# Optimization experiments

Hardware: AMD Instinct MI355X
Metric: run time of the kernel (lower is better)

The kernel has to match this reference:

```python
import jax, jax.numpy as jnp
import numpy as np

N_NODES = 100000
NNZ = 1600000
IN_CH = 256
OUT_CH = 64  # heads * out_channels, heads=1


def setup_inputs() -> dict:
    key = jax.random.key(0)
    k1, k2, k3, k4, k5 = jax.random.split(key, 5)
    X = jax.random.normal(k1, (N_NODES, IN_CH), dtype=jnp.float32)
    # nn.Linear(in, heads*out, bias=False) weight: [out, in]
    W_lin = jax.random.normal(k2, (OUT_CH, IN_CH), dtype=jnp.float32) * (1.0 / np.sqrt(IN_CH))
    # sparse Laplacian L in COO form
    L_rows = jax.random.randint(k3, (NNZ,), 0, N_NODES, dtype=jnp.int64)
    L_cols = jax.random.randint(k4, (NNZ,), 0, N_NODES, dtype=jnp.int64)
    L_vals = jax.random.uniform(k5, (NNZ,), dtype=jnp.float32)
    return {"g1": 0, "g2": 0, "X": X, "W_lin": W_lin,
            "L_rows": L_rows, "L_cols": L_cols, "L_vals": L_vals}


def reference(g1, g2, X, W_lin, L_rows, L_cols, L_vals):
    # dense projection: X @ W^T  -> [N, out]
    Xp = jnp.einsum('ni,oi->no', X, W_lin)
    # SpMM: Xv = L @ Xp, COO gather-scale-scatter
    gathered = L_vals[:, None] * Xp[L_cols]            # [nnz, out]
    Xv = jax.ops.segment_sum(gathered, L_rows, num_segments=N_NODES)
    return Xv
```

## Files before the change

### kernel.cpp

```cpp
#include <hip/hip_runtime.h>

#define N_IN_CH 256
#define N_OUT_CH 64
#define XPAD 264
#define BROW 128
#define NBK 1024
#define B1_T 256
#define B1_E 2048
#define ECAP 4096
#define OVFCAP 65536
#define NGEMM 512

typedef __attribute__((ext_vector_type(8))) short short8;
typedef __attribute__((ext_vector_type(4))) float f32x4;

__device__ inline ushort f2bf(float f) {
    unsigned u = __float_as_uint(f);
    return (ushort)((u + 0x7FFFu + ((u >> 16) & 1u)) >> 16);
}
__device__ inline float bf2f(ushort u) {
    return __uint_as_float(((unsigned)u) << 16);
}

__global__ __launch_bounds__(256) void fused_kernel(const float* __restrict__ X,
        const float* __restrict__ W, ushort* __restrict__ Xp, int nrows, int ngemm,
        const int* __restrict__ rows, const int* __restrict__ cols,
        const float* __restrict__ vals, int* __restrict__ bcur,
        int* __restrict__ ovfcnt, int4* __restrict__ ovf,
        int2* __restrict__ colbuf, int nnz, int nb) {
    __shared__ union SM {
        ushort ws[64 * XPAD];
        struct { int cnt[NBK]; int base[NBK]; } b;
    } sm;
    const int tid = threadIdx.x;

    if (blockIdx.x < ngemm) {
        #pragma unroll
        for (int it = 0; it < 16; ++it) {
            int f = it * 256 + tid;
            int n = f >> 6, c4 = f & 63;
            float4 w = *(const float4*)&W[n * N_IN_CH + c4 * 4];
            ushort4 u;
            u.x = f2bf(w.x); u.y = f2bf(w.y); u.z = f2bf(w.z); u.w = f2bf(w.w);
            *(ushort4*)&sm.ws[n * XPAD + c4 * 4] = u;
        }
        __syncthreads();

        const int wave = tid >> 6, lane = tid & 63;
        const int ml = lane & 15, q = lane >> 4;
        const int ntiles = (nrows + 15) >> 4;
        const int nw = ngemm * 4;
        int t = blockIdx.x * 4 + wave;

        const ushort* wsb = &sm.ws[ml * XPAD + q * 8];

        float4 raw[16];

#define ISSUE_TILE(tt)                                                     \
        do {                                                               \
            int gr_ = (tt) * 16 + ml;                                      \
            if (gr_ < nrows) {                                             \
                const float* xr_ = X + (size_t)gr_ * N_IN_CH + q * 8;      \
                _Pragma("unroll")                                          \
                for (int kt_ = 0; kt_ < 8; ++kt_) {                        \
                    raw[2 * kt_]     = *(const float4*)&xr_[kt_ * 32];     \
                    raw[2 * kt_ + 1] = *(const float4*)&xr_[kt_ * 32 + 4]; \
                }                                                          \
            } else {                                                       \
                _Pragma("unroll")                                          \
                for (int i_ = 0; i_ < 16; ++i_)                            \
                    raw[i_] = make_float4(0.f, 0.f, 0.f, 0.f);             \
            }                                                              \
        } while (0)

        if (t < ntiles) ISSUE_TILE(t);

        while (t < ntiles) {
            short8 a[8];
            #pragma unroll
            for (int kt = 0; kt < 8; ++kt) {
                float4 f0 = raw[2 * kt], f1 = raw[2 * kt + 1];
                short8 s;
                s[0] = (short)f2bf(f0.x); s[1] = (short)f2bf(f0.y);
                s[2] = (short)f2bf(f0.z); s[3] = (short)f2bf(f0.w);
                s[4] = (short)f2bf(f1.x); s[5] = (short)f2bf(f1.y);
                s[6] = (short)f2bf(f1.z); s[7] = (short)f2bf(f1.w);
                a[kt] = s;
            }
            int tn = t + nw;
            if (tn < ntiles) ISSUE_TILE(tn);

            #pragma unroll
            for (int nt = 0; nt < 4; ++nt) {
                f32x4 acc = {0.f, 0.f, 0.f, 0.f};
                #pragma unroll
                for (int kt = 0; kt < 8; ++kt) {
                    short8 b = *(const short8*)&wsb[nt * 16 * XPAD + kt * 32];
                    acc = __builtin_amdgcn_mfma_f32_16x16x32_bf16(a[kt], b, acc, 0, 0, 0);
                }
                #pragma unroll
                for (int reg = 0; reg < 4; ++reg) {
                    int gr = t * 16 + q * 4 + reg;
                    if (gr < nrows)
                        Xp[(size_t)gr * N_OUT_CH + nt * 16 + ml] = f2bf(acc[reg]);
                }
            }
            t = tn;
        }
#undef ISSUE_TILE
    } else {
        for (int i = tid; i < nb; i += B1_T) sm.b.cnt[i] = 0;
        __syncthreads();

        const int e = (blockIdx.x - ngemm) * B1_E + tid * 8;
        int nval = nnz - e;
        if (nval > 8) nval = 8;
        if (nval < 0) nval = 0;

        int r[8], c[8]; float v[8];
        if (nval == 8) {
            *(int4*)&r[0] = *(const int4*)&rows[e];
            *(int4*)&r[4] = *(const int4*)&rows[e + 4];
            *(int4*)&c[0] = *(const int4*)&cols[e];
            *(int4*)&c[4] = *(const int4*)&cols[e + 4];
            *(float4*)&v[0] = *(const float4*)&vals[e];
            *(float4*)&v[4] = *(const float4*)&vals[e + 4];
        } else {
            #pragma unroll
            for (int j = 0; j < 8; ++j)
                if (j < nval) { r[j] = rows[e + j]; c[j] = cols[e + j]; v[j] = vals[e + j]; }
        }

        #pragma unroll
        for (int j = 0; j < 8; ++j)
            if (j < nval) atomicAdd(&sm.b.cnt[r[j] >> 7], 1);
        __syncthreads();

        for (int i = tid; i < nb; i += B1_T) {
            int cn = sm.b.cnt[i];
            sm.b.base[i] = cn ? atomicAdd(&bcur[i], cn) : 0;
            sm.b.cnt[i] = 0;
        }
        __syncthreads();

        #pragma unroll
        for (int j = 0; j < 8; ++j) {
            if (j < nval) {
                int b = r[j] >> 7;
                int pib = sm.b.base[b] + atomicAdd(&sm.b.cnt[b], 1);
                if (pib < ECAP) {
                    int2 cv;
                    cv.x = c[j] | ((r[j] & 127) << 17);
                    cv.y = __float_as_int(v[j]);
                    colbuf[(size_t)b * ECAP + pib] = cv;
                } else {
                    int op = atomicAdd(ovfcnt, 1);
                    if (op < OVFCAP) {
                        int4 o; o.x = r[j]; o.y = c[j];
                        o.z = __float_as_int(v[j]); o.w = 0;
                        ovf[op] = o;
                    }
                }
            }
        }
    }
}

__global__ __launch_bounds__(512) void bspmm_kernel(const int* __restrict__ bcur,
        const int2* __restrict__ colbuf, const ushort* __restrict__ Xp,
        float* __restrict__ out, int nrows, const int* __restrict__ ovfcnt,
        const int4* __restrict__ ovf) {
    __shared__ int2 ebuf[ECAP];
    __shared__ int rc[BROW];
    __shared__ int rb[BROW + 1];
    const int b = blockIdx.x, t = threadIdx.x;
    const int ne = min(bcur[b], ECAP);
    const int2* cb = colbuf + (size_t)b * ECAP;
    const int row0 = b * BROW;

    int2 ev[8];
    const int ebase = t * 8;
    int ecnt = ne - ebase;
    if (ecnt > 8) ecnt = 8;
    if (ecnt < 0) ecnt = 0;
    if (ecnt == 8) {
        #pragma unroll
        for (int j = 0; j < 4; ++j)
            *(int4*)&ev[2 * j] = *(const int4*)&cb[ebase + 2 * j];
    } else {
        #pragma unroll
        for (int j = 0; j < 8; ++j)
            if (j < ecnt) ev[j] = cb[ebase + j];
    }

    if (t < BROW) rc[t] = 0;
    __syncthreads();
    #pragma unroll
    for (int j = 0; j < 8; ++j)
        if (j < ecnt) atomicAdd(&rc[(ev[j].x >> 17) & (BROW - 1)], 1);
    __syncthreads();
    int c0 = (t < BROW) ? rc[t] : 0;
    #pragma unroll
    for (int d = 1; d < BROW; d <<= 1) {
        int a = (t < BROW && t >= d) ? rc[t - d] : 0;
        __syncthreads();
        if (t < BROW) rc[t] += a;
        __syncthreads();
    }
    if (t < BROW) rb[t] = rc[t] - c0;
    if (t == 0) rb[BROW] = ne;
    __syncthreads();
    if (t < BROW) rc[t] = 0;
    __syncthreads();
    #pragma unroll
    for (int j = 0; j < 8; ++j) {
        if (j < ecnt) {
            int rl = (ev[j].x >> 17) & (BROW - 1);
            int pos = rb[rl] + atomicAdd(&rc[rl], 1);
            ebuf[pos] = ev[j];
        }
    }
    __syncthreads();

    const int wave = t >> 6;
    const int q4 = (t >> 4) & 3;
    const int l16 = t & 15;
    const int qr0 = wave * 16 + q4 * 4;
    int i = rb[qr0];
    const int e = rb[qr0 + 4];
    float4 acc = make_float4(0.f, 0.f, 0.f, 0.f);
    int cur = -1;

    for (; i + 4 <= e; i += 4) {
        int2 cv[4];
        #pragma unroll
        for (int j = 0; j < 4; ++j) cv[j] = ebuf[i + j];
        ushort4 xv[4];
        #pragma unroll
        for (int j = 0; j < 4; ++j)
            xv[j] = *(const ushort4*)&Xp[(size_t)(cv[j].x & 0x1FFFF) * N_OUT_CH + l16 * 4];
        #pragma unroll
        for (int j = 0; j < 4; ++j) {
            int rl = (cv[j].x >> 17) & (BROW - 1);
            if (rl != cur) {
                if (cur >= 0)
                    *(float4*)&out[(size_t)(row0 + cur) * N_OUT_CH + l16 * 4] = acc;
                cur = rl;
                acc = make_float4(0.f, 0.f, 0.f, 0.f);
            }
            float vv = __int_as_float(cv[j].y);
            acc.x += vv * bf2f(xv[j].x);
            acc.y += vv * bf2f(xv[j].y);
            acc.z += vv * bf2f(xv[j].z);
            acc.w += vv * bf2f(xv[j].w);
        }
    }
    for (; i < e; ++i) {
        int2 cv = ebuf[i];
        int rl = (cv.x >> 17) & (BROW - 1);
        if (rl != cur) {
            if (cur >= 0)
                *(float4*)&out[(size_t)(row0 + cur) * N_OUT_CH + l16 * 4] = acc;
            cur = rl;
            acc = make_float4(0.f, 0.f, 0.f, 0.f);
        }
        ushort4 xv = *(const ushort4*)&Xp[(size_t)(cv.x & 0x1FFFF) * N_OUT_CH + l16 * 4];
        float vv = __int_as_float(cv.y);
        acc.x += vv * bf2f(xv.x);
        acc.y += vv * bf2f(xv.y);
        acc.z += vv * bf2f(xv.z);
        acc.w += vv * bf2f(xv.w);
    }
    if (cur >= 0)
        *(float4*)&out[(size_t)(row0 + cur) * N_OUT_CH + l16 * 4] = acc;

    #pragma unroll
    for (int r = 0; r < 4; ++r) {
        int lr = qr0 + r;
        if (rb[lr] == rb[lr + 1]) {
            int gr = row0 + lr;
            if (gr < nrows)
                *(float4*)&out[(size_t)gr * N_OUT_CH + l16 * 4] =
                    make_float4(0.f, 0.f, 0.f, 0.f);
        }
    }

    __syncthreads();
    const int lane = t & 63;
    int n = min(ovfcnt[0], OVFCAP);
    for (int e2 = wave; e2 < n; e2 += 8) {
        int4 v = ovf[e2];
        if ((v.x >> 7) == b)
            atomicAdd(&out[(size_t)v.x * N_OUT_CH + lane],
                      __int_as_float(v.z) * bf2f(Xp[(size_t)v.y * N_OUT_CH + lane]));
    }
}

__global__ __launch_bounds__(256) void spmm_atomic_kernel(const int* __restrict__ rows,
        const int* __restrict__ cols, const float* __restrict__ vals,
        const ushort* __restrict__ Xp, float* __restrict__ out, int nnz) {
    int t = blockIdx.x * blockDim.x + threadIdx.x;
    int e = t >> 6;
    int c = t & 63;
    if (e < nnz) {
        atomicAdd(&out[(size_t)rows[e] * N_OUT_CH + c],
                  vals[e] * bf2f(Xp[(size_t)cols[e] * N_OUT_CH + c]));
    }
}

extern "C" void kernel_launch(void* const* d_in, const int* in_sizes, int n_in,
                              void* d_out, int out_size, void* d_ws, size_t ws_size,
                              hipStream_t stream) {
    const float* X      = (const float*)d_in[2];
    const float* W      = (const float*)d_in[3];
    const int*   L_rows = (const int*)d_in[4];
    const int*   L_cols = (const int*)d_in[5];
    const float* L_vals = (const float*)d_in[6];
    float* out = (float*)d_out;

    const int nrows = in_sizes[2] / N_IN_CH;
    const int nnz   = in_sizes[4];
    const int nb    = (nrows + BROW - 1) / BROW;

    size_t off_xp  = 0;
    size_t xp_b    = (size_t)nrows * N_OUT_CH * 2;
    size_t off_bc  = off_xp + ((xp_b + 15) & ~(size_t)15);
    size_t off_ov  = off_bc + (((size_t)(nb + 1) * 4 + 15) & ~(size_t)15);
    size_t off_cv  = off_ov + (size_t)OVFCAP * 16;
    size_t need    = off_cv + (size_t)nb * ECAP * 8;

    ushort* Xp = (ushort*)((char*)d_ws + off_xp);
    const bool binned = (ws_size >= need && nb <= NBK);
    int* bcur = (int*)((char*)d_ws + off_bc);

    int ntiles = (nrows + 15) >> 4;
    int ngemm = NGEMM;
    int maxg = (ntiles + 3) / 4;
    if (ngemm > maxg) ngemm = maxg;

    if (binned) {
        int*  ovfcnt = bcur + nb;
        int4* ovf    = (int4*)((char*)d_ws + off_ov);
        int2* colbuf = (int2*)((char*)d_ws + off_cv);
        int nbin = (nnz + B1_E - 1) / B1_E;

        hipMemsetAsync(bcur, 0, (size_t)(nb + 1) * 4, stream);
        fused_kernel<<<ngemm + nbin, 256, 0, stream>>>(X, W, Xp, nrows, ngemm,
                L_rows, L_cols, L_vals, bcur, ovfcnt, ovf, colbuf, nnz, nb);
        bspmm_kernel<<<nb, 512, 0, stream>>>(bcur, colbuf, Xp, out, nrows, ovfcnt, ovf);
    } else {
        fused_kernel<<<ngemm, 256, 0, stream>>>(X, W, Xp, nrows, ngemm,
                nullptr, nullptr, nullptr, nullptr, nullptr, nullptr, nullptr, 0, 0);
        hipMemsetAsync(d_out, 0, (size_t)out_size * sizeof(float), stream);
        long long total = (long long)nnz * 64;
        spmm_atomic_kernel<<<(int)((total + 255) / 256), 256, 0, stream>>>(
            L_rows, L_cols, L_vals, Xp, out, nnz);
    }
}
```

Measured before the change: 242.0 us.

## Swizzle LDS weights, interleave prefetch with MFMA, widen binning and gather batches

The bf16 weight tile in shared memory drops its row padding and uses an XOR swizzle to avoid bank conflicts. The GEMM loop now issues the next tile's X loads per k-step, interleaved with MFMAs that keep four accumulators. The binning phase handles 16 edges per thread instead of 8, and the SpMM inner loop gathers 8 edges per batch instead of 4, raising memory-level parallelism at the cost of more registers. Launch bounds now request 4 blocks per CU.

After: 287.4 us. 18.7% more time.

```diff
diff --git a/kernel.cpp b/kernel.cpp
--- a/kernel.cpp
+++ b/kernel.cpp
@@ -2,11 +2,11 @@
 
 #define N_IN_CH 256
 #define N_OUT_CH 64
-#define XPAD 264
 #define BROW 128
 #define NBK 1024
 #define B1_T 256
-#define B1_E 2048
+#define B1_PT 16
+#define B1_E 4096
 #define ECAP 4096
 #define OVFCAP 65536
 #define NGEMM 512
@@ -22,14 +22,14 @@
     return __uint_as_float(((unsigned)u) << 16);
 }
 
-__global__ __launch_bounds__(256) void fused_kernel(const float* __restrict__ X,
+__global__ __launch_bounds__(256, 4) void fused_kernel(const float* __restrict__ X,
         const float* __restrict__ W, ushort* __restrict__ Xp, int nrows, int ngemm,
         const int* __restrict__ rows, const int* __restrict__ cols,
         const float* __restrict__ vals, int* __restrict__ bcur,
         int* __restrict__ ovfcnt, int4* __restrict__ ovf,
         int2* __restrict__ colbuf, int nnz, int nb) {
     __shared__ union SM {
-        ushort ws[64 * XPAD];
+        ushort ws[64 * 256];
         struct { int cnt[NBK]; int base[NBK]; } b;
     } sm;
     const int tid = threadIdx.x;
@@ -42,41 +42,47 @@
             float4 w = *(const float4*)&W[n * N_IN_CH + c4 * 4];
             ushort4 u;
             u.x = f2bf(w.x); u.y = f2bf(w.y); u.z = f2bf(w.z); u.w = f2bf(w.w);
-            *(ushort4*)&sm.ws[n * XPAD + c4 * 4] = u;
+            int byteoff = (n << 9) | (((c4 << 3)) ^ ((n & 7) << 4));
+            *(ushort4*)((char*)sm.ws + byteoff) = u;
         }
         __syncthreads();
 
         const int wave = tid >> 6, lane = tid & 63;
         const int ml = lane & 15, q = lane >> 4;
+        const int swz = (ml & 7) << 4;
+        const int q16 = q << 4;
         const int ntiles = (nrows + 15) >> 4;
         const int nw = ngemm * 4;
         int t = blockIdx.x * 4 + wave;
 
-        const ushort* wsb = &sm.ws[ml * XPAD + q * 8];
-
+        const char* wsb = (const char*)sm.ws;
         float4 raw[16];
 
-#define ISSUE_TILE(tt)                                                     \
-        do {                                                               \
-            int gr_ = (tt) * 16 + ml;                                      \
-            if (gr_ < nrows) {                                             \
-                const float* xr_ = X + (size_t)gr_ * N_IN_CH + q * 8;      \
-                _Pragma("unroll")                                          \
-                for (int kt_ = 0; kt_ < 8; ++kt_) {                        \
-                    raw[2 * kt_]     = *(const float4*)&xr_[kt_ * 32];     \
-                    raw[2 * kt_ + 1] = *(const float4*)&xr_[kt_ * 32 + 4]; \
-                }                                                          \
-            } else {                                                       \
-                _Pragma("unroll")                                          \
-                for (int i_ = 0; i_ < 16; ++i_)                            \
-                    raw[i_] = make_float4(0.f, 0.f, 0.f, 0.f);             \
-            }                                                              \
-        } while (0)
-
-        if (t < ntiles) ISSUE_TILE(t);
+        if (t < ntiles) {
+            int gr0 = t * 16 + ml;
+            if (gr0 < nrows) {
+                const float* xr = X + (size_t)gr0 * N_IN_CH + q * 8;
+                #pragma unroll
+                for (int kt = 0; kt < 8; ++kt) {
+                    raw[2 * kt]     = *(const float4*)&xr[kt * 32];
+                    raw[2 * kt + 1] = *(const float4*)&xr[kt * 32 + 4];
+                }
+            } else {
+                #pragma unroll
+                for (int i = 0; i < 16; ++i) raw[i] = make_float4(0.f, 0.f, 0.f, 0.f);
+            }
+        }
 
         while (t < ntiles) {
-            short8 a[8];
+            const int tn = t + nw;
+            const int grn = tn * 16 + ml;
+            const bool okn = grn < nrows;
+            const float* xrn = X + (size_t)grn * N_IN_CH + q * 8;
+
+            f32x4 acc[4];
+            #pragma unroll
+            for (int nt = 0; nt < 4; ++nt) acc[nt] = (f32x4){0.f, 0.f, 0.f, 0.f};
+
             #pragma unroll
             for (int kt = 0; kt < 8; ++kt) {
                 float4 f0 = raw[2 * kt], f1 = raw[2 * kt + 1];
@@ -85,54 +91,59 @@
                 s[2] = (short)f2bf(f0.z); s[3] = (short)f2bf(f0.w);
                 s[4] = (short)f2bf(f1.x); s[5] = (short)f2bf(f1.y);
                 s[6] = (short)f2bf(f1.z); s[7] = (short)f2bf(f1.w);
-                a[kt] = s;
-            }
-            int tn = t + nw;
-            if (tn < ntiles) ISSUE_TILE(tn);
+                if (tn < ntiles) {
+                    if (okn) {
+                        raw[2 * kt]     = *(const float4*)&xrn[kt * 32];
+                        raw[2 * kt + 1] = *(const float4*)&xrn[kt * 32 + 4];
+                    } else {
+                        raw[2 * kt]     = make_float4(0.f, 0.f, 0.f, 0.f);
+                        raw[2 * kt + 1] = make_float4(0.f, 0.f, 0.f, 0.f);
+                    }
+                }
+                #pragma unroll
+                for (int nt = 0; nt < 4; ++nt) {
+                    short8 b = *(const short8*)(wsb + ((nt * 16 + ml) << 9)
+                                                + (((kt << 6) | q16) ^ swz));
+                    acc[nt] = __builtin_amdgcn_mfma_f32_16x16x32_bf16(s, b, acc[nt], 0, 0, 0);
+                }
+            }
 
             #pragma unroll
             for (int nt = 0; nt < 4; ++nt) {
-                f32x4 acc = {0.f, 0.f, 0.f, 0.f};
-                #pragma unroll
-                for (int kt = 0; kt < 8; ++kt) {
-                    short8 b = *(const short8*)&wsb[nt * 16 * XPAD + kt * 32];
-                    acc = __builtin_amdgcn_mfma_f32_16x16x32_bf16(a[kt], b, acc, 0, 0, 0);
-                }
                 #pragma unroll
                 for (int reg = 0; reg < 4; ++reg) {
                     int gr = t * 16 + q * 4 + reg;
                     if (gr < nrows)
-                        Xp[(size_t)gr * N_OUT_CH + nt * 16 + ml] = f2bf(acc[reg]);
+                        Xp[(size_t)gr * N_OUT_CH + nt * 16 + ml] = f2bf(acc[nt][reg]);
                 }
             }
             t = tn;
         }
-#undef ISSUE_TILE
     } else {
         for (int i = tid; i < nb; i += B1_T) sm.b.cnt[i] = 0;
         __syncthreads();
 
-        const int e = (blockIdx.x - ngemm) * B1_E + tid * 8;
+        const int e = (blockIdx.x - ngemm) * B1_E + tid * B1_PT;
         int nval = nnz - e;
-        if (nval > 8) nval = 8;
+        if (nval > B1_PT) nval = B1_PT;
         if (nval < 0) nval = 0;
 
-        int r[8], c[8]; float v[8];
-        if (nval == 8) {
-            *(int4*)&r[0] = *(const int4*)&rows[e];
-            *(int4*)&r[4] = *(const int4*)&rows[e + 4];
-            *(int4*)&c[0] = *(const int4*)&cols[e];
-            *(int4*)&c[4] = *(const int4*)&cols[e + 4];
-            *(float4*)&v[0] = *(const float4*)&vals[e];
-            *(float4*)&v[4] = *(const float4*)&vals[e + 4];
+        int r[B1_PT], c[B1_PT]; float v[B1_PT];
+        if (nval == B1_PT) {
+            #pragma unroll
+            for (int j = 0; j < B1_PT / 4; ++j) {
+                *(int4*)&r[4 * j] = *(const int4*)&rows[e + 4 * j];
+                *(int4*)&c[4 * j] = *(const int4*)&cols[e + 4 * j];
+                *(float4*)&v[4 * j] = *(const float4*)&vals[e + 4 * j];
+            }
         } else {
             #pragma unroll
-            for (int j = 0; j < 8; ++j)
+            for (int j = 0; j < B1_PT; ++j)
                 if (j < nval) { r[j] = rows[e + j]; c[j] = cols[e + j]; v[j] = vals[e + j]; }
         }
 
         #pragma unroll
-        for (int j = 0; j < 8; ++j)
+        for (int j = 0; j < B1_PT; ++j)
             if (j < nval) atomicAdd(&sm.b.cnt[r[j] >> 7], 1);
         __syncthreads();
 
@@ -144,7 +155,7 @@
         __syncthreads();
 
         #pragma unroll
-        for (int j = 0; j < 8; ++j) {
+        for (int j = 0; j < B1_PT; ++j) {
             if (j < nval) {
                 int b = r[j] >> 7;
                 int pib = sm.b.base[b] + atomicAdd(&sm.b.cnt[b], 1);
@@ -231,16 +242,16 @@
     float4 acc = make_float4(0.f, 0.f, 0.f, 0.f);
     int cur = -1;
 
-    for (; i + 4 <= e; i += 4) {
-        int2 cv[4];
-        #pragma unroll
-        for (int j = 0; j < 4; ++j) cv[j] = ebuf[i + j];
-        ushort4 xv[4];
-        #pragma unroll
-        for (int j = 0; j < 4; ++j)
+    for (; i + 8 <= e; i += 8) {
+        int2 cv[8];
+        #pragma unroll
+        for (int j = 0; j < 8; ++j) cv[j] = ebuf[i + j];
+        ushort4 xv[8];
+        #pragma unroll
+        for (int j = 0; j < 8; ++j)
             xv[j] = *(const ushort4*)&Xp[(size_t)(cv[j].x & 0x1FFFF) * N_OUT_CH + l16 * 4];
         #pragma unroll
-        for (int j = 0; j < 4; ++j) {
+        for (int j = 0; j < 8; ++j) {
             int rl = (cv[j].x >> 17) & (BROW - 1);
             if (rl != cur) {
                 if (cur >= 0)
```
